# Kernel tuning notes

Measured on AMD Instinct MI355X. Metric: run time of the kernel, lower is better.

Reference implementation:

```python
import jax, jax.numpy as jnp
import numpy as np

EMBED_DIM = 768
NUM_HEADS = 8
HEAD_DIM = EMBED_DIM // NUM_HEADS
WINDOW_HALF = (17 - 1) // 2          # window_size=17 -> 8
GAP = 3 + 1                          # dilation_gap=3 -> stride 4
OVERLAP = WINDOW_HALF * GAP          # 32
N_LINES = 8192


def setup_inputs() -> dict:
    key = jax.random.key(0)
    k1, k2, k3, k4, k5 = jax.random.split(key, 5)
    D = EMBED_DIM
    return {
        "main": jax.random.normal(k1, (N_LINES, D), dtype=jnp.float32),
        "begin": jax.random.normal(k2, (OVERLAP, D), dtype=jnp.float32),
        "end": jax.random.normal(k3, (OVERLAP, D), dtype=jnp.float32),
        "in_proj_w": jax.random.normal(k4, (3 * D, D), dtype=jnp.float32) * 0.02,
        "in_proj_b": jnp.zeros((3 * D,), dtype=jnp.float32),
        "out_proj_w": jax.random.normal(k5, (D, D), dtype=jnp.float32) * 0.02,
        "out_proj_b": jnp.zeros((D,), dtype=jnp.float32),
    }


def reference(main, begin, end, in_proj_w, in_proj_b, out_proj_w, out_proj_b):
    N, D = main.shape
    H, hd = NUM_HEADS, HEAD_DIM
    # combined buffer [begin | main | end]; the per-token shifted concatenations
    # in the torch loop are equivalent to a strided gather into this buffer.
    combined = jnp.concatenate([begin, main, end], axis=0)  # [N + 2*OVERLAP, D]
    offsets = jnp.concatenate([
        jnp.arange(-OVERLAP, 0, GAP),
        jnp.arange(GAP, OVERLAP + GAP, GAP),
    ])  # [2*WINDOW_HALF] = [16]
    idx = jnp.arange(N)[:, None] + OVERLAP + offsets[None, :]  # [N, W]
    keys = combined[idx]  # [N, W, D] dilated window keys (= values)

    wq, wk, wv = in_proj_w[:D], in_proj_w[D:2 * D], in_proj_w[2 * D:]
    bq, bk, bv = in_proj_b[:D], in_proj_b[D:2 * D], in_proj_b[2 * D:]

    q = (main @ wq.T + bq).reshape(N, H, hd) * (hd ** -0.5)   # [N,H,hd]
    k = (keys @ wk.T + bk).reshape(N, -1, H, hd)              # [N,W,H,hd]
    v = (keys @ wv.T + bv).reshape(N, -1, H, hd)              # [N,W,H,hd]

    scores = jnp.einsum('nhd,nwhd->nhw', q, k)                # [N,H,W]
    attn = jax.nn.softmax(scores, axis=-1)
    ctx = jnp.einsum('nhw,nwhd->nhd', attn, v).reshape(N, D)
    attn_out = ctx @ out_proj_w.T + out_proj_b                # [N,D]
    return jnp.concatenate([main, attn_out], axis=-1)         # [N,2D]
```

## Files before the change

kernel.cpp:

```cpp
#include <hip/hip_runtime.h>
#include <math.h>

#define D 768
#define NQKV 2304
#define NH 8
#define HD 96
#define NW 16
#define OVL 32
#define NLINES 8192
#define NCOMB 8256
#define MPAD 8320
#define CH 64
#define SCALE_Q 0.1020620726159657f

typedef int i32x8 __attribute__((ext_vector_type(8)));
typedef float f32x4 __attribute__((ext_vector_type(4)));

__device__ __forceinline__ unsigned short f2bf(float f) {
    unsigned int u = __float_as_uint(f);
    u += 0x7FFF + ((u >> 16) & 1);
    return (unsigned short)(u >> 16);
}
__device__ __forceinline__ float bflo(unsigned int u) { return __uint_as_float(u << 16); }
__device__ __forceinline__ float bfhi(unsigned int u) { return __uint_as_float(u & 0xFFFF0000u); }

__device__ __forceinline__ void stage16(const void* g, void* l) {
    __builtin_amdgcn_global_load_lds(
        (const __attribute__((address_space(1))) unsigned int*)g,
        (__attribute__((address_space(3))) unsigned int*)l, 16, 0, 0);
}

__device__ __forceinline__ unsigned int pk_fp8x4(float a, float b, float c, float d) {
    int u = __builtin_amdgcn_cvt_pk_fp8_f32(a, b, 0, false);
    u = __builtin_amdgcn_cvt_pk_fp8_f32(c, d, u, true);
    return (unsigned int)u;
}


__global__ __launch_bounds__(256) void convert_comb(const float* __restrict__ main_,
                                                    const float* __restrict__ begin_,
                                                    const float* __restrict__ end_,
                                                    unsigned int* __restrict__ dst) {
    const int i = blockIdx.x * 256 + threadIdx.x;
    const int row = i / 192;
    const int c4 = i % 192;
    float4 v = make_float4(0.f, 0.f, 0.f, 0.f);
    if (row < NCOMB) {
        const float* src = (row < OVL) ? begin_ + (size_t)row * D
                         : (row < OVL + NLINES) ? main_ + (size_t)(row - OVL) * D
                                                : end_ + (size_t)(row - OVL - NLINES) * D;
        v = *(const float4*)(src + c4 * 4);
    }
    dst[(size_t)row * 192 + c4] = pk_fp8x4(v.x, v.y, v.z, v.w);
}

__global__ __launch_bounds__(256) void convert_w(const float* __restrict__ in_w,
                                                 const float* __restrict__ in_b,
                                                 const float* __restrict__ out_w,
                                                 unsigned int* __restrict__ w_dst,
                                                 float* __restrict__ bias_s) {
    const int i = blockIdx.x * 256 + threadIdx.x;
    const int f0 = i * 4;
    const bool is_out = f0 >= 3 * D * D;
    const float4 v = is_out ? *(const float4*)(out_w + (f0 - 3 * D * D))
                            : *(const float4*)(in_w + f0);
    const float s = 16.0f * ((f0 < D * D) ? SCALE_Q : 1.0f);
    w_dst[i] = pk_fp8x4(v.x * s, v.y * s, v.z * s, v.w * s);
    if (blockIdx.x == 0) {
        for (int b = threadIdx.x; b < NQKV; b += 256)
            bias_s[b] = in_b[b] * (b < D ? SCALE_Q : 1.0f);
    }
}

__device__ __forceinline__ void gemm_f8_loop(const unsigned char* __restrict__ A,
                                             const unsigned char* __restrict__ B,
                                             unsigned char* As, unsigned char* Bs,
                                             int m0, int n0, f32x4 (&acc)[4][4]) {
    const int tid = threadIdx.x;
    const int lane = tid & 63;
    const int wave = tid >> 6;
    const int wm = (wave & 1) * 64;
    const int wn = (wave >> 1) * 64;
    const int q = lane >> 4;
    const int l15 = lane & 15;

    for (int k0 = 0; k0 < D; k0 += 128) {
#pragma unroll
        for (int it = 0; it < 4; it++) {
            const int ch = tid + it * 256;
            const int row = ch >> 3, c16 = (ch & 7) * 16;
            stage16(A + (size_t)(m0 + row) * D + k0 + c16, As + ch * 16);
            stage16(B + (size_t)(n0 + row) * D + k0 + c16, Bs + ch * 16);
        }
        __syncthreads();
        i32x8 af[4], bfr[4];
#pragma unroll
        for (int i = 0; i < 4; i++)
            af[i] = *(const i32x8*)(As + (wm + i * 16 + l15) * 128 + q * 32);
#pragma unroll
        for (int j = 0; j < 4; j++)
            bfr[j] = *(const i32x8*)(Bs + (wn + j * 16 + l15) * 128 + q * 32);
#pragma unroll
        for (int i = 0; i < 4; i++)
#pragma unroll
            for (int j = 0; j < 4; j++)
                acc[i][j] = __builtin_amdgcn_mfma_scale_f32_16x16x128_f8f6f4(
                    af[i], bfr[j], acc[i][j],  0,  0,
                     0,  127,  0,  123);
        __syncthreads();
    }
}

__global__ __launch_bounds__(256) void qkv_gemm(const unsigned char* __restrict__ comb,
                                                const unsigned char* __restrict__ w_f8,
                                                const float* __restrict__ bias_s,
                                                unsigned short* __restrict__ Qb,
                                                unsigned short* __restrict__ Kb,
                                                unsigned short* __restrict__ Vb) {
    __shared__ __align__(16) unsigned char As[128 * 128];
    __shared__ __align__(16) unsigned char Bs[128 * 128];
    const int bx = blockIdx.x;
    const int m0 = blockIdx.y * 128;
    f32x4 acc[4][4] = {};
    gemm_f8_loop(comb, w_f8, As, Bs, m0, bx * 128, acc);

    const int lane = threadIdx.x & 63;
    const int wave = threadIdx.x >> 6;
    const int wm = (wave & 1) * 64, wn = (wave >> 1) * 64;
    const int q = lane >> 4, l15 = lane & 15;
    unsigned short* Cb = (bx < 6) ? Qb : (bx < 12 ? Kb : Vb);
    const int nloc = (bx % 6) * 128;
#pragma unroll
    for (int i = 0; i < 4; i++)
#pragma unroll
        for (int j = 0; j < 4; j++)
#pragma unroll
            for (int r = 0; r < 4; r++) {
                const int row = m0 + wm + i * 16 + q * 4 + r;
                const int col = wn + j * 16 + l15;
                const float v = acc[i][j][r] + bias_s[bx * 128 + col];
                Cb[(size_t)row * D + nloc + col] = f2bf(v);
            }
}

__global__ __launch_bounds__(256) void out_gemm(const unsigned char* __restrict__ ctx,
                                                const unsigned char* __restrict__ w,
                                                const float* __restrict__ bias,
                                                const float* __restrict__ main_,
                                                float* __restrict__ out) {
    __shared__ __align__(16) unsigned char As[128 * 128];
    __shared__ __align__(16) unsigned char Bs[128 * 128];
    const int m0 = blockIdx.y * 128;
    const int n0 = blockIdx.x * 128;
    f32x4 acc[4][4] = {};
    gemm_f8_loop(ctx, w, As, Bs, m0, n0, acc);

    const int tid = threadIdx.x;
    const int lane = tid & 63;
    const int wave = tid >> 6;
    const int wm = (wave & 1) * 64, wn = (wave >> 1) * 64;
    const int q = lane >> 4, l15 = lane & 15;
#pragma unroll
    for (int i = 0; i < 4; i++)
#pragma unroll
        for (int j = 0; j < 4; j++)
#pragma unroll
            for (int r = 0; r < 4; r++) {
                const int row = m0 + wm + i * 16 + q * 4 + r;
                const int col = n0 + wn + j * 16 + l15;
                out[(size_t)row * (2 * D) + D + col] = acc[i][j][r] + bias[col];
            }
#pragma unroll
    for (int it = 0; it < 16; it++) {
        const int idx = tid + it * 256;
        const int r = idx >> 5, c4 = idx & 31;
        const float4 v = *(const float4*)(main_ + (size_t)(m0 + r) * D + n0 + c4 * 4);
        *(float4*)(out + (size_t)(m0 + r) * (2 * D) + n0 + c4 * 4) = v;
    }
}

__global__ __launch_bounds__(256) void attn_kernel(const unsigned short* __restrict__ Q,
                                                   const unsigned short* __restrict__ K,
                                                   const unsigned short* __restrict__ V,
                                                   unsigned char* __restrict__ ctx) {
    const int n0 = blockIdx.x * CH;
    const int h = blockIdx.y;
    const int tid = threadIdx.x;

    __shared__ __align__(16) unsigned short sQ[CH * 104];
    __shared__ __align__(16) unsigned short sK[128 * 104];
    __shared__ __align__(16) unsigned short sV[128 * 104];
    __shared__ float sS[CH][17];

#pragma unroll
    for (int it = 0; it < 3; it++) {
        const int idx = tid + it * 256;
        const int row = idx / 12, c = idx % 12;
        *(uint4*)(sQ + row * 104 + c * 8) =
            *(const uint4*)(Q + (size_t)(n0 + row) * D + h * HD + c * 8);
    }
#pragma unroll
    for (int it = 0; it < 6; it++) {
        const int idx = tid + it * 256;
        const int row = idx / 12, c = idx % 12;
        *(uint4*)(sK + row * 104 + c * 8) =
            *(const uint4*)(K + (size_t)(n0 + row) * D + h * HD + c * 8);
        *(uint4*)(sV + row * 104 + c * 8) =
            *(const uint4*)(V + (size_t)(n0 + row) * D + h * HD + c * 8);
    }
    __syncthreads();

    const int l = tid & 63;
    const int wg = tid >> 6;

    uint4 qreg[12];
#pragma unroll
    for (int c = 0; c < 12; c++) qreg[c] = *(const uint4*)(sQ + l * 104 + c * 8);
#pragma unroll
    for (int wi = 0; wi < 4; wi++) {
        const int w = wg * 4 + wi;
        const int lrow = l + 4 * w + (w >= 8 ? 4 : 0);
        float s = 0.f;
#pragma unroll
        for (int c = 0; c < 12; c++) {
            const uint4 kv = *(const uint4*)(sK + lrow * 104 + c * 8);
            s += bflo(qreg[c].x) * bflo(kv.x) + bfhi(qreg[c].x) * bfhi(kv.x);
            s += bflo(qreg[c].y) * bflo(kv.y) + bfhi(qreg[c].y) * bfhi(kv.y);
            s += bflo(qreg[c].z) * bflo(kv.z) + bfhi(qreg[c].z) * bfhi(kv.z);
            s += bflo(qreg[c].w) * bflo(kv.w) + bfhi(qreg[c].w) * bfhi(kv.w);
        }
        sS[l][w] = s;
    }
    __syncthreads();

    if (tid < CH) {
        float mx = -1e30f;
#pragma unroll
        for (int i = 0; i < NW; i++) mx = fmaxf(mx, sS[tid][i]);
        float e[NW], sum = 0.f;
#pragma unroll
        for (int i = 0; i < NW; i++) {
            e[i] = __expf(sS[tid][i] - mx);
            sum += e[i];
        }
        const float inv = 1.f / sum;
#pragma unroll
        for (int i = 0; i < NW; i++) sS[tid][i] = e[i] * inv;
    }
    __syncthreads();

    float p[NW];
#pragma unroll
    for (int i = 0; i < NW; i++) p[i] = sS[l][i];
    float acc[24] = {};
#pragma unroll
    for (int i = 0; i < NW; i++) {
        const int lrow = l + 4 * i + (i >= 8 ? 4 : 0);
        const unsigned short* vp = sV + lrow * 104 + wg * 24;
        const float pw = p[i];
#pragma unroll
        for (int c = 0; c < 3; c++) {
            const uint4 vv = *(const uint4*)(vp + c * 8);
            acc[c * 8 + 0] += pw * bflo(vv.x);
            acc[c * 8 + 1] += pw * bfhi(vv.x);
            acc[c * 8 + 2] += pw * bflo(vv.y);
            acc[c * 8 + 3] += pw * bfhi(vv.y);
            acc[c * 8 + 4] += pw * bflo(vv.z);
            acc[c * 8 + 5] += pw * bfhi(vv.z);
            acc[c * 8 + 6] += pw * bflo(vv.w);
            acc[c * 8 + 7] += pw * bfhi(vv.w);
        }
    }
    unsigned char* op = ctx + (size_t)(n0 + l) * D + h * HD + wg * 24;
#pragma unroll
    for (int c = 0; c < 3; c++) {
        const unsigned int u0 = pk_fp8x4(acc[c * 8 + 0], acc[c * 8 + 1], acc[c * 8 + 2], acc[c * 8 + 3]);
        const unsigned int u1 = pk_fp8x4(acc[c * 8 + 4], acc[c * 8 + 5], acc[c * 8 + 6], acc[c * 8 + 7]);
        *(uint2*)(op + c * 8) = make_uint2(u0, u1);
    }
}

extern "C" void kernel_launch(void* const* d_in, const int* in_sizes, int n_in,
                              void* d_out, int out_size, void* d_ws, size_t ws_size,
                              hipStream_t stream) {
    const float* main_ = (const float*)d_in[0];
    const float* begin_ = (const float*)d_in[1];
    const float* end_ = (const float*)d_in[2];
    const float* in_w = (const float*)d_in[3];
    const float* in_b = (const float*)d_in[4];
    const float* out_w = (const float*)d_in[5];
    const float* out_b = (const float*)d_in[6];
    float* out = (float*)d_out;

    unsigned char* comb_f8 = (unsigned char*)d_ws;
    unsigned char* w_f8 = comb_f8 + (size_t)MPAD * D;
    unsigned short* Qb = (unsigned short*)(w_f8 + (size_t)4 * D * D);
    unsigned short* Kb = Qb + (size_t)MPAD * D;
    unsigned short* Vb = Kb + (size_t)MPAD * D;
    unsigned char* ctx_f8 = (unsigned char*)(Vb + (size_t)MPAD * D);
    float* bias_s = (float*)(ctx_f8 + (size_t)NLINES * D);

    convert_comb<<<MPAD * 192 / 256, 256, 0, stream>>>(main_, begin_, end_,
                                                       (unsigned int*)comb_f8);
    convert_w<<<4 * D * D / 1024, 256, 0, stream>>>(in_w, in_b, out_w,
                                                    (unsigned int*)w_f8, bias_s);
    qkv_gemm<<<dim3(NQKV / 128, MPAD / 128), 256, 0, stream>>>(comb_f8, w_f8, bias_s,
                                                               Qb, Kb, Vb);
    attn_kernel<<<dim3(NLINES / CH, NH), 256, 0, stream>>>(Qb + (size_t)OVL * D, Kb, Vb,
                                                           ctx_f8);
    out_gemm<<<dim3(D / 128, NLINES / 128), 256, 0, stream>>>(ctx_f8, w_f8 + (size_t)3 * D * D,
                                                              out_b, main_, out);
}
```

Before: 176.1 us.

## Store QKV in fp8, fuse conversion kernels, swizzle LDS, shrink out_gemm tile

Q, K and V are now written as fp8 instead of bf16, which halves the intermediate traffic between the QKV GEMM and the attention kernel, and attention unpacks them with hardware fp8 conversions. The two conversion kernels are merged into one launch. The GEMM LDS staging uses an XOR-style column swizzle to avoid bank conflicts. out_gemm moves to 64-row tiles so more blocks are launched. The lower-precision Q/K/V adds more rounding error to the attention scores.

```diff
diff --git a/kernel.cpp b/kernel.cpp
--- a/kernel.cpp
+++ b/kernel.cpp
@@ -12,17 +12,29 @@
 #define MPAD 8320
 #define CH 64
 #define SCALE_Q 0.1020620726159657f
+#define COMB_BLOCKS 6240
 
 typedef int i32x8 __attribute__((ext_vector_type(8)));
 typedef float f32x4 __attribute__((ext_vector_type(4)));
-
-__device__ __forceinline__ unsigned short f2bf(float f) {
-    unsigned int u = __float_as_uint(f);
-    u += 0x7FFF + ((u >> 16) & 1);
-    return (unsigned short)(u >> 16);
-}
-__device__ __forceinline__ float bflo(unsigned int u) { return __uint_as_float(u << 16); }
-__device__ __forceinline__ float bfhi(unsigned int u) { return __uint_as_float(u & 0xFFFF0000u); }
+typedef float f32x2 __attribute__((ext_vector_type(2)));
+
+__device__ __forceinline__ unsigned int pk_fp8x4(float a, float b, float c, float d) {
+    int u = __builtin_amdgcn_cvt_pk_fp8_f32(a, b, 0, false);
+    u = __builtin_amdgcn_cvt_pk_fp8_f32(c, d, u, true);
+    return (unsigned int)u;
+}
+__device__ __forceinline__ unsigned char f2fp8(float v) {
+    return (unsigned char)(__builtin_amdgcn_cvt_pk_fp8_f32(v, v, 0, false) & 0xFF);
+}
+template <bool HI>
+__device__ __forceinline__ f32x2 upk(unsigned int u) {
+    return __builtin_amdgcn_cvt_pk_f32_fp8((int)u, HI);
+}
+__device__ __forceinline__ float dot4f8(unsigned int a, unsigned int b) {
+    const f32x2 al = upk<false>(a), ah = upk<true>(a);
+    const f32x2 bl = upk<false>(b), bh = upk<true>(b);
+    return al.x * bl.x + al.y * bl.y + ah.x * bh.x + ah.y * bh.y;
+}
 
 __device__ __forceinline__ void stage16(const void* g, void* l) {
     __builtin_amdgcn_global_load_lds(
@@ -30,105 +42,93 @@
         (__attribute__((address_space(3))) unsigned int*)l, 16, 0, 0);
 }
 
-__device__ __forceinline__ unsigned int pk_fp8x4(float a, float b, float c, float d) {
-    int u = __builtin_amdgcn_cvt_pk_fp8_f32(a, b, 0, false);
-    u = __builtin_amdgcn_cvt_pk_fp8_f32(c, d, u, true);
-    return (unsigned int)u;
-}
-
-
-__global__ __launch_bounds__(256) void convert_comb(const float* __restrict__ main_,
-                                                    const float* __restrict__ begin_,
-                                                    const float* __restrict__ end_,
-                                                    unsigned int* __restrict__ dst) {
-    const int i = blockIdx.x * 256 + threadIdx.x;
-    const int row = i / 192;
-    const int c4 = i % 192;
-    float4 v = make_float4(0.f, 0.f, 0.f, 0.f);
-    if (row < NCOMB) {
-        const float* src = (row < OVL) ? begin_ + (size_t)row * D
-                         : (row < OVL + NLINES) ? main_ + (size_t)(row - OVL) * D
-                                                : end_ + (size_t)(row - OVL - NLINES) * D;
-        v = *(const float4*)(src + c4 * 4);
-    }
-    dst[(size_t)row * 192 + c4] = pk_fp8x4(v.x, v.y, v.z, v.w);
-}
-
-__global__ __launch_bounds__(256) void convert_w(const float* __restrict__ in_w,
-                                                 const float* __restrict__ in_b,
-                                                 const float* __restrict__ out_w,
-                                                 unsigned int* __restrict__ w_dst,
-                                                 float* __restrict__ bias_s) {
-    const int i = blockIdx.x * 256 + threadIdx.x;
-    const int f0 = i * 4;
-    const bool is_out = f0 >= 3 * D * D;
-    const float4 v = is_out ? *(const float4*)(out_w + (f0 - 3 * D * D))
-                            : *(const float4*)(in_w + f0);
-    const float s = 16.0f * ((f0 < D * D) ? SCALE_Q : 1.0f);
-    w_dst[i] = pk_fp8x4(v.x * s, v.y * s, v.z * s, v.w * s);
-    if (blockIdx.x == 0) {
-        for (int b = threadIdx.x; b < NQKV; b += 256)
-            bias_s[b] = in_b[b] * (b < D ? SCALE_Q : 1.0f);
-    }
-}
-
-__device__ __forceinline__ void gemm_f8_loop(const unsigned char* __restrict__ A,
-                                             const unsigned char* __restrict__ B,
-                                             unsigned char* As, unsigned char* Bs,
-                                             int m0, int n0, f32x4 (&acc)[4][4]) {
-    const int tid = threadIdx.x;
-    const int lane = tid & 63;
-    const int wave = tid >> 6;
-    const int wm = (wave & 1) * 64;
-    const int wn = (wave >> 1) * 64;
-    const int q = lane >> 4;
-    const int l15 = lane & 15;
-
-    for (int k0 = 0; k0 < D; k0 += 128) {
-#pragma unroll
-        for (int it = 0; it < 4; it++) {
-            const int ch = tid + it * 256;
-            const int row = ch >> 3, c16 = (ch & 7) * 16;
-            stage16(A + (size_t)(m0 + row) * D + k0 + c16, As + ch * 16);
-            stage16(B + (size_t)(n0 + row) * D + k0 + c16, Bs + ch * 16);
-        }
-        __syncthreads();
-        i32x8 af[4], bfr[4];
-#pragma unroll
-        for (int i = 0; i < 4; i++)
-            af[i] = *(const i32x8*)(As + (wm + i * 16 + l15) * 128 + q * 32);
-#pragma unroll
-        for (int j = 0; j < 4; j++)
-            bfr[j] = *(const i32x8*)(Bs + (wn + j * 16 + l15) * 128 + q * 32);
-#pragma unroll
-        for (int i = 0; i < 4; i++)
-#pragma unroll
-            for (int j = 0; j < 4; j++)
-                acc[i][j] = __builtin_amdgcn_mfma_scale_f32_16x16x128_f8f6f4(
-                    af[i], bfr[j], acc[i][j],  0,  0,
-                     0,  127,  0,  123);
-        __syncthreads();
+__device__ __forceinline__ void stage_sw(const unsigned char* gbase, unsigned char* lds, int ch) {
+    const int row = ch >> 3;
+    const int half = ch & 1;
+    const int o = (((ch >> 1) & 3) - row) & 3;
+    stage16(gbase + (size_t)row * D + o * 32 + half * 16, lds + ch * 16);
+}
+
+__global__ __launch_bounds__(256) void convert_all(const float* __restrict__ main_,
+                                                   const float* __restrict__ begin_,
+                                                   const float* __restrict__ end_,
+                                                   const float* __restrict__ in_w,
+                                                   const float* __restrict__ in_b,
+                                                   const float* __restrict__ out_w,
+                                                   unsigned int* __restrict__ comb_dst,
+                                                   unsigned int* __restrict__ w_dst,
+                                                   float* __restrict__ bias_s) {
+    const int bid = blockIdx.x;
+    if (bid < COMB_BLOCKS) {
+        const int i = bid * 256 + threadIdx.x;
+        const int row = i / 192, c4 = i % 192;
+        float4 v = make_float4(0.f, 0.f, 0.f, 0.f);
+        if (row < NCOMB) {
+            const float* src = (row < OVL) ? begin_ + (size_t)row * D
+                             : (row < OVL + NLINES) ? main_ + (size_t)(row - OVL) * D
+                                                    : end_ + (size_t)(row - OVL - NLINES) * D;
+            v = *(const float4*)(src + c4 * 4);
+        }
+        comb_dst[(size_t)row * 192 + c4] = pk_fp8x4(v.x, v.y, v.z, v.w);
+    } else {
+        const int j = (bid - COMB_BLOCKS) * 256 + threadIdx.x;
+        const int f0 = j * 4;
+        const bool is_out = f0 >= 3 * D * D;
+        const float4 v = is_out ? *(const float4*)(out_w + (f0 - 3 * D * D))
+                                : *(const float4*)(in_w + f0);
+        const float s = 16.0f * ((f0 < D * D) ? SCALE_Q : 1.0f);
+        w_dst[j] = pk_fp8x4(v.x * s, v.y * s, v.z * s, v.w * s);
+        if (bid == COMB_BLOCKS) {
+            for (int b = threadIdx.x; b < NQKV; b += 256)
+                bias_s[b] = in_b[b] * (b < D ? SCALE_Q : 1.0f);
+        }
     }
 }
 
 __global__ __launch_bounds__(256) void qkv_gemm(const unsigned char* __restrict__ comb,
                                                 const unsigned char* __restrict__ w_f8,
                                                 const float* __restrict__ bias_s,
-                                                unsigned short* __restrict__ Qb,
-                                                unsigned short* __restrict__ Kb,
-                                                unsigned short* __restrict__ Vb) {
+                                                unsigned char* __restrict__ Qb,
+                                                unsigned char* __restrict__ Kb,
+                                                unsigned char* __restrict__ Vb) {
     __shared__ __align__(16) unsigned char As[128 * 128];
     __shared__ __align__(16) unsigned char Bs[128 * 128];
     const int bx = blockIdx.x;
     const int m0 = blockIdx.y * 128;
-    f32x4 acc[4][4] = {};
-    gemm_f8_loop(comb, w_f8, As, Bs, m0, bx * 128, acc);
-
-    const int lane = threadIdx.x & 63;
-    const int wave = threadIdx.x >> 6;
+    const int n0 = bx * 128;
+    const int tid = threadIdx.x;
+    const int lane = tid & 63;
+    const int wave = tid >> 6;
     const int wm = (wave & 1) * 64, wn = (wave >> 1) * 64;
     const int q = lane >> 4, l15 = lane & 15;
-    unsigned short* Cb = (bx < 6) ? Qb : (bx < 12 ? Kb : Vb);
+    const int swq = (q + l15) & 3;
+
+    f32x4 acc[4][4] = {};
+    for (int k0 = 0; k0 < D; k0 += 128) {
+#pragma unroll
+        for (int it = 0; it < 4; it++) {
+            const int ch = tid + it * 256;
+            stage_sw(comb + (size_t)m0 * D + k0, As, ch);
+            stage_sw(w_f8 + (size_t)n0 * D + k0, Bs, ch);
+        }
+        __syncthreads();
+        i32x8 af[4], bfr[4];
+#pragma unroll
+        for (int i = 0; i < 4; i++)
+            af[i] = *(const i32x8*)(As + (wm + i * 16 + l15) * 128 + swq * 32);
+#pragma unroll
+        for (int j = 0; j < 4; j++)
+            bfr[j] = *(const i32x8*)(Bs + (wn + j * 16 + l15) * 128 + swq * 32);
+#pragma unroll
+        for (int i = 0; i < 4; i++)
+#pragma unroll
+            for (int j = 0; j < 4; j++)
+                acc[i][j] = __builtin_amdgcn_mfma_scale_f32_16x16x128_f8f6f4(
+                    af[i], bfr[j], acc[i][j], 0, 0, 0, 127, 0, 123);
+        __syncthreads();
+    }
+
+    unsigned char* Cb = (bx < 6) ? Qb : (bx < 12 ? Kb : Vb);
     const int nloc = (bx % 6) * 128;
 #pragma unroll
     for (int i = 0; i < 4; i++)
@@ -138,8 +138,7 @@
             for (int r = 0; r < 4; r++) {
                 const int row = m0 + wm + i * 16 + q * 4 + r;
                 const int col = wn + j * 16 + l15;
-                const float v = acc[i][j][r] + bias_s[bx * 128 + col];
-                Cb[(size_t)row * D + nloc + col] = f2bf(v);
+                Cb[(size_t)row * D + nloc + col] = f2fp8(acc[i][j][r] + bias_s[bx * 128 + col]);
             }
 }
 
@@ -148,30 +147,54 @@
                                                 const float* __restrict__ bias,
                                                 const float* __restrict__ main_,
                                                 float* __restrict__ out) {
-    __shared__ __align__(16) unsigned char As[128 * 128];
+    __shared__ __align__(16) unsigned char As[64 * 128];
     __shared__ __align__(16) unsigned char Bs[128 * 128];
-    const int m0 = blockIdx.y * 128;
+    const int m0 = blockIdx.y * 64;
     const int n0 = blockIdx.x * 128;
-    f32x4 acc[4][4] = {};
-    gemm_f8_loop(ctx, w, As, Bs, m0, n0, acc);
-
     const int tid = threadIdx.x;
     const int lane = tid & 63;
     const int wave = tid >> 6;
-    const int wm = (wave & 1) * 64, wn = (wave >> 1) * 64;
+    const int wn = wave * 32;
     const int q = lane >> 4, l15 = lane & 15;
+    const int swq = (q + l15) & 3;
+
+    f32x4 acc[4][2] = {};
+    for (int k0 = 0; k0 < D; k0 += 128) {
+#pragma unroll
+        for (int it = 0; it < 2; it++)
+            stage_sw(ctx + (size_t)m0 * D + k0, As, tid + it * 256);
+#pragma unroll
+        for (int it = 0; it < 4; it++)
+            stage_sw(w + (size_t)n0 * D + k0, Bs, tid + it * 256);
+        __syncthreads();
+        i32x8 af[4], bfr[2];
+#pragma unroll
+        for (int i = 0; i < 4; i++)
+            af[i] = *(const i32x8*)(As + (i * 16 + l15) * 128 + swq * 32);
+#pragma unroll
+        for (int j = 0; j < 2; j++)
+            bfr[j] = *(const i32x8*)(Bs + (wn + j * 16 + l15) * 128 + swq * 32);
+#pragma unroll
+        for (int i = 0; i < 4; i++)
+#pragma unroll
+            for (int j = 0; j < 2; j++)
+                acc[i][j] = __builtin_amdgcn_mfma_scale_f32_16x16x128_f8f6f4(
+                    af[i], bfr[j], acc[i][j], 0, 0, 0, 127, 0, 123);
+        __syncthreads();
+    }
+
 #pragma unroll
     for (int i = 0; i < 4; i++)
 #pragma unroll
-        for (int j = 0; j < 4; j++)
+        for (int j = 0; j < 2; j++)
 #pragma unroll
             for (int r = 0; r < 4; r++) {
-                const int row = m0 + wm + i * 16 + q * 4 + r;
+                const int row = m0 + i * 16 + q * 4 + r;
                 const int col = n0 + wn + j * 16 + l15;
                 out[(size_t)row * (2 * D) + D + col] = acc[i][j][r] + bias[col];
             }
 #pragma unroll
-    for (int it = 0; it < 16; it++) {
+    for (int it = 0; it < 8; it++) {
         const int idx = tid + it * 256;
         const int r = idx >> 5, c4 = idx & 31;
         const float4 v = *(const float4*)(main_ + (size_t)(m0 + r) * D + n0 + c4 * 4);
@@ -179,55 +202,49 @@
     }
 }
 
-__global__ __launch_bounds__(256) void attn_kernel(const unsigned short* __restrict__ Q,
-                                                   const unsigned short* __restrict__ K,
-                                                   const unsigned short* __restrict__ V,
+__global__ __launch_bounds__(256) void attn_kernel(const unsigned char* __restrict__ Q,
+                                                   const unsigned char* __restrict__ K,
+                                                   const unsigned char* __restrict__ V,
                                                    unsigned char* __restrict__ ctx) {
     const int n0 = blockIdx.x * CH;
     const int h = blockIdx.y;
     const int tid = threadIdx.x;
 
-    __shared__ __align__(16) unsigned short sQ[CH * 104];
-    __shared__ __align__(16) unsigned short sK[128 * 104];
-    __shared__ __align__(16) unsigned short sV[128 * 104];
+    __shared__ __align__(16) unsigned char sQ[CH * 96];
+    __shared__ __align__(16) unsigned char sK[128 * 96];
+    __shared__ __align__(16) unsigned char sV[128 * 96];
     __shared__ float sS[CH][17];
 
+    for (int idx = tid; idx < 384; idx += 256) {
+        const int row = idx / 6, c = idx % 6;
+        *(uint4*)(sQ + row * 96 + c * 16) =
+            *(const uint4*)(Q + (size_t)(n0 + row) * D + h * HD + c * 16);
+    }
 #pragma unroll
     for (int it = 0; it < 3; it++) {
         const int idx = tid + it * 256;
-        const int row = idx / 12, c = idx % 12;
-        *(uint4*)(sQ + row * 104 + c * 8) =
-            *(const uint4*)(Q + (size_t)(n0 + row) * D + h * HD + c * 8);
-    }
-#pragma unroll
-    for (int it = 0; it < 6; it++) {
-        const int idx = tid + it * 256;
-        const int row = idx / 12, c = idx % 12;
-        *(uint4*)(sK + row * 104 + c * 8) =
-            *(const uint4*)(K + (size_t)(n0 + row) * D + h * HD + c * 8);
-        *(uint4*)(sV + row * 104 + c * 8) =
-            *(const uint4*)(V + (size_t)(n0 + row) * D + h * HD + c * 8);
+        const int row = idx / 6, c = idx % 6;
+        *(uint4*)(sK + row * 96 + c * 16) =
+            *(const uint4*)(K + (size_t)(n0 + row) * D + h * HD + c * 16);
+        *(uint4*)(sV + row * 96 + c * 16) =
+            *(const uint4*)(V + (size_t)(n0 + row) * D + h * HD + c * 16);
     }
     __syncthreads();
 
     const int l = tid & 63;
     const int wg = tid >> 6;
 
-    uint4 qreg[12];
-#pragma unroll
-    for (int c = 0; c < 12; c++) qreg[c] = *(const uint4*)(sQ + l * 104 + c * 8);
 #pragma unroll
     for (int wi = 0; wi < 4; wi++) {
         const int w = wg * 4 + wi;
         const int lrow = l + 4 * w + (w >= 8 ? 4 : 0);
         float s = 0.f;
 #pragma unroll
-        for (int c = 0; c < 12; c++) {
-            const uint4 kv = *(const uint4*)(sK + lrow * 104 + c * 8);
-            s += bflo(qreg[c].x) * bflo(kv.x) + bfhi(qreg[c].x) * bfhi(kv.x);
-            s += bflo(qreg[c].y) * bflo(kv.y) + bfhi(qreg[c].y) * bfhi(kv.y);
-            s += bflo(qreg[c].z) * bflo(kv.z) + bfhi(qreg[c].z) * bfhi(kv.z);
-            s += bflo(qreg[c].w) * bflo(kv.w) + bfhi(qreg[c].w) * bfhi(kv.w);
+        for (int c = 0; c < 6; c++) {
+            const uint4 qa = *(const uint4*)(sQ + l * 96 + c * 16);
+            const uint4 ka = *(const uint4*)(sK + lrow * 96 + c * 16);
+            s += dot4f8(qa.x, ka.x) + dot4f8(qa.y, ka.y) +
+                 dot4f8(qa.z, ka.z) + dot4f8(qa.w, ka.w);
         }
         sS[l][w] = s;
     }
@@ -256,26 +273,30 @@
 #pragma unroll
     for (int i = 0; i < NW; i++) {
         const int lrow = l + 4 * i + (i >= 8 ? 4 : 0);
-        const unsigned short* vp = sV + lrow * 104 + wg * 24;
+        const unsigned char* vp = sV + lrow * 96 + wg * 24;
         const float pw = p[i];
 #pragma unroll
         for (int c = 0; c < 3; c++) {
-            const uint4 vv = *(const uint4*)(vp + c * 8);
-            acc[c * 8 + 0] += pw * bflo(vv.x);
-            acc[c * 8 + 1] += pw * bfhi(vv.x);
-            acc[c * 8 + 2] += pw * bflo(vv.y);
-            acc[c * 8 + 3] += pw * bfhi(vv.y);
-            acc[c * 8 + 4] += pw * bflo(vv.z);
-            acc[c * 8 + 5] += pw * bfhi(vv.z);
-            acc[c * 8 + 6] += pw * bflo(vv.w);
-            acc[c * 8 + 7] += pw * bfhi(vv.w);
+            const uint2 vv = *(const uint2*)(vp + c * 8);
+            const f32x2 a0 = upk<false>(vv.x), a1 = upk<true>(vv.x);
+            const f32x2 a2 = upk<false>(vv.y), a3 = upk<true>(vv.y);
+            acc[c * 8 + 0] += pw * a0.x;
+            acc[c * 8 + 1] += pw * a0.y;
+            acc[c * 8 + 2] += pw * a1.x;
+            acc[c * 8 + 3] += pw * a1.y;
+            acc[c * 8 + 4] += pw * a2.x;
+            acc[c * 8 + 5] += pw * a2.y;
+            acc[c * 8 + 6] += pw * a3.x;
+            acc[c * 8 + 7] += pw * a3.y;
         }
     }
     unsigned char* op = ctx + (size_t)(n0 + l) * D + h * HD + wg * 24;
 #pragma unroll
     for (int c = 0; c < 3; c++) {
-        const unsigned int u0 = pk_fp8x4(acc[c * 8 + 0], acc[c * 8 + 1], acc[c * 8 + 2], acc[c * 8 + 3]);
-        const unsigned int u1 = pk_fp8x4(acc[c * 8 + 4], acc[c * 8 + 5], acc[c * 8 + 6], acc[c * 8 + 7]);
+        const unsigned int u0 =
+            pk_fp8x4(acc[c * 8 + 0], acc[c * 8 + 1], acc[c * 8 + 2], acc[c * 8 + 3]);
+        const unsigned int u1 =
+            pk_fp8x4(acc[c * 8 + 4], acc[c * 8 + 5], acc[c * 8 + 6], acc[c * 8 + 7]);
         *(uint2*)(op + c * 8) = make_uint2(u0, u1);
     }
 }
@@ -294,20 +315,19 @@
 
     unsigned char* comb_f8 = (unsigned char*)d_ws;
     unsigned char* w_f8 = comb_f8 + (size_t)MPAD * D;
-    unsigned short* Qb = (unsigned short*)(w_f8 + (size_t)4 * D * D);
-    unsigned short* Kb = Qb + (size_t)MPAD * D;
-    unsigned short* Vb = Kb + (size_t)MPAD * D;
-    unsigned char* ctx_f8 = (unsigned char*)(Vb + (size_t)MPAD * D);
+    unsigned char* Qb = w_f8 + (size_t)4 * D * D;
+    unsigned char* Kb = Qb + (size_t)MPAD * D;
+    unsigned char* Vb = Kb + (size_t)MPAD * D;
+    unsigned char* ctx_f8 = Vb + (size_t)MPAD * D;
     float* bias_s = (float*)(ctx_f8 + (size_t)NLINES * D);
 
-    convert_comb<<<MPAD * 192 / 256, 256, 0, stream>>>(main_, begin_, end_,
-                                                       (unsigned int*)comb_f8);
-    convert_w<<<4 * D * D / 1024, 256, 0, stream>>>(in_w, in_b, out_w,
-                                                    (unsigned int*)w_f8, bias_s);
+    convert_all<<<COMB_BLOCKS + 4 * D * D / 1024, 256, 0, stream>>>(
+        main_, begin_, end_, in_w, in_b, out_w, (unsigned int*)comb_f8,
+        (unsigned int*)w_f8, bias_s);
     qkv_gemm<<<dim3(NQKV / 128, MPAD / 128), 256, 0, stream>>>(comb_f8, w_f8, bias_s,
                                                                Qb, Kb, Vb);
     attn_kernel<<<dim3(NLINES / CH, NH), 256, 0, stream>>>(Qb + (size_t)OVL * D, Kb, Vb,
                                                            ctx_f8);
-    out_gemm<<<dim3(D / 128, NLINES / 128), 256, 0, stream>>>(ctx_f8, w_f8 + (size_t)3 * D * D,
-                                                              out_b, main_, out);
-}
+    out_gemm<<<dim3(D / 128, NLINES / 64), 256, 0, stream>>>(ctx_f8, w_f8 + (size_t)3 * D * D,
+                                                             out_b, main_, out);
+}
```

Measured after the change: 164.7 us. -6.5%, faster.
